# Performance work log

Hardware: AMD Instinct MI355X
Metric: run time of the kernel (lower is better)

Reference implementation:

```python
import jax, jax.numpy as jnp
import numpy as np
import math

N0, E, D_IN, H, NC, UH = 4096, 65536, 128, 256, 10, 64
K1 = math.ceil(0.8 * N0)   # 3277 nodes kept by pool1
K2 = math.ceil(0.2 * K1)   # 656 nodes kept by pool2

PARAM_SHAPES = dict(
    gcn1_w=(D_IN, H), gcn1_b=(H,), pool1_w=(H,), gcn2_w=(H, H), gcn2_b=(H,), pool2_w=(H,),
    inr_w=(H, H), inr_b=(H,), ini_w=(H, H), ini_b=(H,),
    enc1_w=(1, UH), enc1_b=(UH,), enc2_w=(UH, UH), enc2_b=(UH,),
    p1_w=(UH, UH), p1_b=(UH,), p2_w=(UH, UH // 2), p2_b=(UH // 2,),
    p3_w=(UH // 2, K2 * K2), p3_b=(K2 * K2,),
    rt_w=(H, H), rt_b=(H,), it_w=(H, H), it_b=(H,),
    msg_wr=(H, H), msg_wi=(H, H),
    mc1_w=(H, H // 2), mc1_b=(H // 2,), mc2_w=(H // 2, NC), mc2_b=(NC,),
    pc1_w=(H, H // 2), pc1_b=(H // 2,), pc2_w=(H // 2, NC), pc2_b=(NC,),
)

def gcn_conv(x, src, dst, emask, W, b):
    # GCNConv: self-loops + symmetric normalization; emask zeroes edges dropped by pooling
    n = x.shape[0]
    h = x @ W
    deg = jnp.zeros((n,), h.dtype).at[dst].add(emask) + 1.0
    dis = jax.lax.rsqrt(deg)
    coef = dis[src] * dis[dst] * emask
    out = jnp.zeros_like(h).at[dst].add(coef[:, None] * h[src])
    out = out + (dis * dis)[:, None] * h   # self-loop contribution
    return out + b

def topk_pool(x, src, dst, emask, w, k):
    # PyG TopKPooling: score = x@w/||w||, keep top-k, x <- x[perm]*tanh(score[perm])
    n = x.shape[0]
    score = (x @ w) / jnp.linalg.norm(w)
    _, perm = jax.lax.top_k(score, k)
    x_new = x[perm] * jnp.tanh(score[perm])[:, None]
    mapping = jnp.full((n,), -1, jnp.int32).at[perm].set(jnp.arange(k, dtype=jnp.int32))
    ns, nd = mapping[src], mapping[dst]
    nm = emask * (ns >= 0) * (nd >= 0)
    return x_new, jnp.maximum(ns, 0), jnp.maximum(nd, 0), nm

def herm_sqrt(C):
    C = (C + C.conj().T) * 0.5
    w, V = jnp.linalg.eigh(C)
    w = jnp.maximum(w, 0.0)
    return (V * jnp.sqrt(w + 1e-8)) @ V.conj().T

def forward(x, edge_index, P):
    src, dst = edge_index[0], edge_index[1]
    em = jnp.ones((src.shape[0],), jnp.float32)
    h = jax.nn.relu(gcn_conv(x, src, dst, em, P['gcn1_w'], P['gcn1_b']))
    h, src, dst, em = topk_pool(h, src, dst, em, P['pool1_w'], K1)
    h = jax.nn.relu(gcn_conv(h, src, dst, em, P['gcn2_w'], P['gcn2_b']))
    h, src, dst, em = topk_pool(h, src, dst, em, P['pool2_w'], K2)
    xr = h @ P['inr_w'] + P['inr_b']
    xi = h @ P['ini_w'] + P['ini_b']
    # --- LocalQuantumLayer (eval mode: dropout is identity) ---
    # ImprovedUnitaryDilationNetwork on the pooled graph (N = K2)
    xg = jnp.ones((K2, 1), jnp.float32)
    xg = jax.nn.relu(gcn_conv(xg, src, dst, em, P['enc1_w'], P['enc1_b']))
    xg = gcn_conv(xg, src, dst, em, P['enc2_w'], P['enc2_b'])
    emb = xg.mean(0)                                     # global_mean_pool, single graph
    t = jax.nn.relu(emb @ P['p1_w'] + P['p1_b'])
    t = jax.nn.relu(t @ P['p2_w'] + P['p2_b'])
    pm = jnp.tanh(t @ P['p3_w'] + P['p3_b']).reshape(K2, K2)
    A = 0.05 * ((pm - pm.T) * 0.5 + 1j * (pm + pm.T) * 0.5)  # antihermitian, scaled
    U = jax.scipy.linalg.expm(A)
    I = jnp.eye(K2, dtype=U.dtype)
    S1 = jax.lax.stop_gradient(herm_sqrt(I - U.conj().T @ U))
    S2 = jax.lax.stop_gradient(herm_sqrt(I - U @ U.conj().T))
    U_dil = jnp.concatenate([jnp.concatenate([U, S1], 1),
                             jnp.concatenate([S2, -U.conj().T], 1)], 0)
    xrt = jax.nn.relu(xr @ P['rt_w'] + P['rt_b'])
    xit = jax.nn.relu(xi @ P['it_w'] + P['it_b'])
    xc = xrt + 1j * xit
    # unitary_dim = 2*K2 > K2 nodes -> single batch, U_sub = U_dil[:K2,:K2]
    evolved = U_dil[:K2, :K2] @ xc
    Wm = P['msg_wr'] + 1j * P['msg_wi']
    msg = evolved[src] @ Wm                              # message(x_j) = x_j @ W (complex)
    agg = jnp.zeros_like(xc).at[dst].add(msg * em[:, None])  # aggr='add'
    outc = agg + (xr + 1j * xi)                          # identity residual (dims equal)
    mag = jnp.abs(outc)
    ph = jnp.arctan2(outc.imag, outc.real)
    gm, gp = mag.mean(0), ph.mean(0)                     # global_mean_pool, single graph
    lm = jax.nn.relu(gm @ P['mc1_w'] + P['mc1_b']) @ P['mc2_w'] + P['mc2_b']
    lp = jax.nn.relu(gp @ P['pc1_w'] + P['pc1_b']) @ P['pc2_w'] + P['pc2_b']
    return lm + lp

def setup_inputs() -> dict:
    key = jax.random.key(0)
    ks = iter(jax.random.split(key, 64))
    inp = {}
    inp['x'] = jax.random.normal(next(ks), (N0, D_IN), jnp.float32)
    inp['edge_index'] = jax.random.randint(next(ks), (2, E), 0, N0)
    for name, shp in PARAM_SHAPES.items():
        inp[name] = jax.random.normal(next(ks), shp, jnp.float32) * 0.05
    return inp

def reference(x, edge_index, gcn1_w, gcn1_b, pool1_w, gcn2_w, gcn2_b, pool2_w, inr_w, inr_b, ini_w, ini_b, enc1_w, enc1_b, enc2_w, enc2_b, p1_w, p1_b, p2_w, p2_b, p3_w, p3_b, rt_w, rt_b, it_w, it_b, msg_wr, msg_wi, mc1_w, mc1_b, mc2_w, mc2_b, pc1_w, pc1_b, pc2_w, pc2_b):
    P = dict(locals())
    x_ = P.pop('x'); ei = P.pop('edge_index')
    return forward(x_, ei, P)
```

## Files before the change

kernel.cpp:

```cpp
#include <hip/hip_runtime.h>
#include <cstddef>
#include <utility>

constexpr int N0  = 4096;
constexpr int E   = 65536;
constexpr int DIN = 128;
constexpr int HD  = 256;
constexpr int NC  = 10;
constexpr int UHD = 64;
constexpr int K1  = 3277;
constexpr int K2  = 656;
constexpr int PMN = K2 * K2;

constexpr int SQ_SLOTS = 4;

constexpr int PLD = 704;
constexpr size_t PPS = (size_t)PLD * PLD;

constexpr int CSPLIT = 8;

#define F4(n) ((size_t)(n) * 4)
constexpr size_t O_H1    = 0;
constexpr size_t O_OUT1  = O_H1    + F4(N0 * HD);
constexpr size_t O_DEG1  = O_OUT1  + F4(N0 * HD);
constexpr size_t O_DIS1  = O_DEG1  + F4(N0);
constexpr size_t O_SC1   = O_DIS1  + F4(N0);
constexpr size_t O_PERM1 = O_SC1   + F4(N0);
constexpr size_t O_MAP1  = O_PERM1 + F4(N0);
constexpr size_t O_H1P   = O_MAP1  + F4(N0);
constexpr size_t O_SRC2  = O_H1P   + F4(K1 * HD);
constexpr size_t O_DST2  = O_SRC2  + F4(E);
constexpr size_t O_EM2   = O_DST2  + F4(E);
constexpr size_t O_H2    = O_EM2   + F4(E);
constexpr size_t O_OUT2  = O_H2    + F4(K1 * HD);
constexpr size_t O_DEG2  = O_OUT2  + F4(K1 * HD);
constexpr size_t O_DIS2  = O_DEG2  + F4(N0);
constexpr size_t O_SC2   = O_DIS2  + F4(N0);
constexpr size_t O_PERM2 = O_SC2   + F4(N0);
constexpr size_t O_MAP2  = O_PERM2 + F4(N0);
constexpr size_t O_H2P   = O_MAP2  + F4(N0);
constexpr size_t O_SRC3  = O_H2P   + F4(K2 * HD);
constexpr size_t O_DST3  = O_SRC3  + F4(E);
constexpr size_t O_EM3   = O_DST3  + F4(E);
constexpr size_t O_XR    = O_EM3   + F4(E);
constexpr size_t O_XI    = O_XR    + F4(K2 * HD);
constexpr size_t O_DEG3  = O_XI    + F4(K2 * HD);
constexpr size_t O_DIS3  = O_DEG3  + F4(1024);
constexpr size_t O_SCOEF = O_DIS3  + F4(1024);
constexpr size_t O_XG1   = O_SCOEF + F4(1024);
constexpr size_t O_XG2H  = O_XG1   + F4(K2 * UHD);
constexpr size_t O_XG2   = O_XG2H  + F4(K2 * UHD);
constexpr size_t O_EMB   = O_XG2   + F4(K2 * UHD);
constexpr size_t O_T1    = O_EMB   + F4(64);
constexpr size_t O_T2    = O_T1    + F4(64);
constexpr size_t O_NORM  = O_T2    + F4(64);
constexpr size_t O_PM    = O_NORM  + F4(64);
constexpr size_t O_BM    = O_PM    + F4(PMN);
constexpr size_t O_P0    = O_BM    + F4(PMN) * 2;
constexpr size_t O_P1    = O_P0    + F4(PMN) * 2;
constexpr size_t O_XRT   = O_P1    + F4(PMN) * 2;
constexpr size_t O_XIT   = O_XRT   + F4(K2 * HD);
constexpr size_t O_XC    = O_XIT   + F4(K2 * HD);
constexpr size_t O_EVO   = O_XC    + F4(K2 * HD) * 2;
constexpr size_t O_AGG0  = O_EVO   + F4(K2 * HD) * 2;
constexpr size_t O_WC    = O_AGG0  + F4(K2 * HD) * 2;
constexpr size_t O_AGG1  = O_WC    + F4(HD * HD) * 2;
constexpr size_t O_MAG   = O_AGG1  + F4(K2 * HD) * 2;
constexpr size_t O_PH    = O_MAG   + F4(K2 * HD);
constexpr size_t O_GM    = O_PH    + F4(K2 * HD);
constexpr size_t O_GP    = O_GM    + F4(256);
constexpr size_t O_HM    = O_GP    + F4(256);
constexpr size_t O_HP    = O_HM    + F4(256);
constexpr size_t O_LM    = O_HP    + F4(256);
constexpr size_t O_LP    = O_LM    + F4(64);
constexpr size_t WS_NEED = O_LP    + F4(64);

constexpr size_t O_SA = 0;
constexpr size_t O_ST = O_SA + PPS * 2 * 4;
static_assert(O_ST + PPS * 2 * 4 <= O_SRC3, "SA/ST must fit in dead region");

constexpr size_t O_B2 = O_XRT;
static_assert(O_B2 + F4(PMN) * 2 <= O_MAG, "B2 must fit in XRT..AGG1 region");

constexpr size_t O_CSR_OFF = O_MAG;
constexpr size_t O_CSR_CUR = O_CSR_OFF + F4(4104);
constexpr size_t O_CSR_SRC = O_CSR_CUR + F4(4104);
constexpr size_t O_CSR_CF  = O_CSR_SRC + F4(E);
static_assert(O_CSR_CF + F4(E) <= O_GM, "CSR must fit in MAG/PH region");

constexpr size_t O_PARTX  = (WS_NEED + 255) & ~(size_t)255;
constexpr size_t PART_SZ  = (size_t)CSPLIT * PMN * 8;
constexpr size_t WS_TOTAL = O_PARTX + PART_SZ;

typedef __attribute__((ext_vector_type(8))) short s8v;
typedef __attribute__((ext_vector_type(4))) float f4v;

__device__ inline unsigned short f2bf(float x) {
  unsigned u = __float_as_uint(x);
  u += 0x7FFFu + ((u >> 16) & 1u);
  return (unsigned short)(u >> 16);
}
__device__ inline float bf2f(unsigned short h) {
  return __uint_as_float(((unsigned)h) << 16);
}
__device__ inline void split4(float re, float im, unsigned short* out,
                              size_t ps, size_t o) {
  unsigned short rh = f2bf(re);
  unsigned short rl = f2bf(re - bf2f(rh));
  unsigned short ih = f2bf(im);
  unsigned short il = f2bf(im - bf2f(ih));
  out[o] = rh; out[ps + o] = rl; out[2 * ps + o] = ih; out[3 * ps + o] = il;
}


template <int ACT>
__global__ void rmm64(const float* __restrict__ A, const float* __restrict__ B,
                      const float* __restrict__ bias, float* __restrict__ C,
                      int M, int N, int K, int CS, int CO) {
  __shared__ float As[64][17];
  __shared__ float Bs[16][64];
  int t  = threadIdx.x;
  int tx = t & 15, ty = t >> 4;
  int bm = blockIdx.y * 64, bn = blockIdx.x * 64;
  float ra[4], rb[4];
#pragma unroll
  for (int i = 0; i < 4; i++) {
    int l = t + i * 256;
    int gr = bm + (l >> 4);
    ra[i] = (gr < M) ? A[(size_t)gr * K + (l & 15)] : 0.f;
    int gc = bn + (l & 63);
    rb[i] = (gc < N) ? B[(size_t)(l >> 6) * N + gc] : 0.f;
  }
  float acc[4][4] = {};
  for (int kt = 0; kt < K; kt += 16) {
#pragma unroll
    for (int i = 0; i < 4; i++) {
      int l = t + i * 256;
      As[l >> 4][l & 15] = ra[i];
      Bs[l >> 6][l & 63] = rb[i];
    }
    __syncthreads();
    int kn = kt + 16;
    if (kn < K) {
#pragma unroll
      for (int i = 0; i < 4; i++) {
        int l = t + i * 256;
        int gr = bm + (l >> 4);
        ra[i] = (gr < M) ? A[(size_t)gr * K + kn + (l & 15)] : 0.f;
        int gc = bn + (l & 63);
        rb[i] = (gc < N) ? B[(size_t)(kn + (l >> 6)) * N + gc] : 0.f;
      }
    }
#pragma unroll
    for (int kk = 0; kk < 16; kk++) {
      float a[4], b[4];
#pragma unroll
      for (int i = 0; i < 4; i++) a[i] = As[ty + 16 * i][kk];
#pragma unroll
      for (int j = 0; j < 4; j++) b[j] = Bs[kk][tx + 16 * j];
#pragma unroll
      for (int i = 0; i < 4; i++)
#pragma unroll
        for (int j = 0; j < 4; j++) acc[i][j] += a[i] * b[j];
    }
    __syncthreads();
  }
#pragma unroll
  for (int i = 0; i < 4; i++) {
    int r = bm + ty + 16 * i;
    if (r >= M) continue;
#pragma unroll
    for (int j = 0; j < 4; j++) {
      int c = bn + tx + 16 * j;
      if (c >= N) continue;
      float v = acc[i][j] + (bias ? bias[c] : 0.f);
      if (ACT == 1) v = fmaxf(v, 0.f);
      C[((size_t)r * N + c) * CS + CO] = v;
    }
  }
}

template <int ACT>
__global__ void rmm64_dual(const float* __restrict__ A0, const float* __restrict__ A1,
                           const float* __restrict__ B0, const float* __restrict__ B1,
                           const float* __restrict__ b0, const float* __restrict__ b1,
                           float* __restrict__ C0, float* __restrict__ C1,
                           int M, int N, int K, int CS) {
  const float* A = blockIdx.z ? A1 : A0;
  const float* B = blockIdx.z ? B1 : B0;
  const float* bias = blockIdx.z ? b1 : b0;
  float* C = blockIdx.z ? C1 : C0;
  __shared__ float As[64][17];
  __shared__ float Bs[16][64];
  int t  = threadIdx.x;
  int tx = t & 15, ty = t >> 4;
  int bm = blockIdx.y * 64, bn = blockIdx.x * 64;
  float ra[4], rb[4];
#pragma unroll
  for (int i = 0; i < 4; i++) {
    int l = t + i * 256;
    int gr = bm + (l >> 4);
    ra[i] = (gr < M) ? A[(size_t)gr * K + (l & 15)] : 0.f;
    int gc = bn + (l & 63);
    rb[i] = (gc < N) ? B[(size_t)(l >> 6) * N + gc] : 0.f;
  }
  float acc[4][4] = {};
  for (int kt = 0; kt < K; kt += 16) {
#pragma unroll
    for (int i = 0; i < 4; i++) {
      int l = t + i * 256;
      As[l >> 4][l & 15] = ra[i];
      Bs[l >> 6][l & 63] = rb[i];
    }
    __syncthreads();
    int kn = kt + 16;
    if (kn < K) {
#pragma unroll
      for (int i = 0; i < 4; i++) {
        int l = t + i * 256;
        int gr = bm + (l >> 4);
        ra[i] = (gr < M) ? A[(size_t)gr * K + kn + (l & 15)] : 0.f;
        int gc = bn + (l & 63);
        rb[i] = (gc < N) ? B[(size_t)(kn + (l >> 6)) * N + gc] : 0.f;
      }
    }
#pragma unroll
    for (int kk = 0; kk < 16; kk++) {
      float a[4], b[4];
#pragma unroll
      for (int i = 0; i < 4; i++) a[i] = As[ty + 16 * i][kk];
#pragma unroll
      for (int j = 0; j < 4; j++) b[j] = Bs[kk][tx + 16 * j];
#pragma unroll
      for (int i = 0; i < 4; i++)
#pragma unroll
        for (int j = 0; j < 4; j++) acc[i][j] += a[i] * b[j];
    }
    __syncthreads();
  }
#pragma unroll
  for (int i = 0; i < 4; i++) {
    int r = bm + ty + 16 * i;
    if (r >= M) continue;
#pragma unroll
    for (int j = 0; j < 4; j++) {
      int c = bn + tx + 16 * j;
      if (c >= N) continue;
      float v = acc[i][j] + (bias ? bias[c] : 0.f);
      if (ACT == 1) v = fmaxf(v, 0.f);
      C[((size_t)r * N + c) * CS] = v;
    }
  }
}

__global__ void split_planesT(const float2* __restrict__ in, int inM, int inN,
                              unsigned short* __restrict__ out, int padR, int ld,
                              size_t ps) {
  __shared__ float2 tile[32][33];
  int tx = threadIdx.x & 31, ty = threadIdx.x >> 5;
  int k0 = blockIdx.x * 32, n0 = blockIdx.y * 32;
  for (int i = ty; i < 32; i += 8) {
    int k = k0 + i, n = n0 + tx;
    tile[i][tx] = (k < inM && n < inN) ? in[(size_t)k * inN + n]
                                       : make_float2(0.f, 0.f);
  }
  __syncthreads();
  for (int i = ty; i < 32; i += 8) {
    int n = n0 + i, k = k0 + tx;
    if (n < padR && k < ld)
      split4(tile[tx][i].x, tile[tx][i].y, out, ps, (size_t)n * ld + k);
  }
}

__global__ void split_planesT2(const float* __restrict__ re, const float* __restrict__ im,
                               int inM, int inN, unsigned short* __restrict__ out,
                               int padR, int ld, size_t ps) {
  __shared__ float2 tile[32][33];
  int tx = threadIdx.x & 31, ty = threadIdx.x >> 5;
  int k0 = blockIdx.x * 32, n0 = blockIdx.y * 32;
  for (int i = ty; i < 32; i += 8) {
    int k = k0 + i, n = n0 + tx;
    tile[i][tx] = (k < inM && n < inN)
        ? make_float2(re[(size_t)k * inN + n], im[(size_t)k * inN + n])
        : make_float2(0.f, 0.f);
  }
  __syncthreads();
  for (int i = ty; i < 32; i += 8) {
    int n = n0 + i, k = k0 + tx;
    if (n < padR && k < ld)
      split4(tile[tx][i].x, tile[tx][i].y, out, ps, (size_t)n * ld + k);
  }
}

__global__ __launch_bounds__(256, 2) void cmm_bf16_sk(
    const unsigned short* __restrict__ SA, size_t psA, int ldA,
    const unsigned short* __restrict__ ST, size_t psT, int ldT,
    float2* __restrict__ Part, int M, int N, int Kp, int chunk,
    const int* __restrict__ gate, int slot) {
  if (gate && slot >= *gate - 1) return;
  int k0 = blockIdx.x * chunk;
  int kend = min(Kp, k0 + chunk);
  int t = threadIdx.x;
  int wave = t >> 6, lane = t & 63;
  int quad = lane >> 4, mn = lane & 15;
  int rowA = blockIdx.z * 64 + wave * 16 + mn;
  int bn = blockIdx.y * 64;
  const unsigned short* a0 = SA + (size_t)rowA * ldA;
  f4v accR[4], accI[4];
#pragma unroll
  for (int i = 0; i < 4; i++) {
    accR[i] = (f4v){0.f, 0.f, 0.f, 0.f};
    accI[i] = (f4v){0.f, 0.f, 0.f, 0.f};
  }
  s8v cA[4], cB[4][4], nA[4], nB[4][4];
  {
    int ka = k0 + quad * 8;
#pragma unroll
    for (int p = 0; p < 4; p++) cA[p] = *(const s8v*)(a0 + p * psA + ka);
#pragma unroll
    for (int tl = 0; tl < 4; tl++) {
      const unsigned short* b0 = ST + (size_t)(bn + tl * 16 + mn) * ldT + ka;
#pragma unroll
      for (int p = 0; p < 4; p++) cB[tl][p] = *(const s8v*)(b0 + p * psT);
    }
  }
  for (int kt = k0; kt < kend; kt += 32) {
    int kn = kt + 32;
    if (kn < kend) {
      int ka = kn + quad * 8;
#pragma unroll
      for (int p = 0; p < 4; p++) nA[p] = *(const s8v*)(a0 + p * psA + ka);
#pragma unroll
      for (int tl = 0; tl < 4; tl++) {
        const unsigned short* b0 = ST + (size_t)(bn + tl * 16 + mn) * ldT + ka;
#pragma unroll
        for (int p = 0; p < 4; p++) nB[tl][p] = *(const s8v*)(b0 + p * psT);
      }
    }
    s8v nih, nil_;
#pragma unroll
    for (int q = 0; q < 8; q++) {
      nih[q]  = (short)(cA[2][q] ^ (short)0x8000);
      nil_[q] = (short)(cA[3][q] ^ (short)0x8000);
    }
#pragma unroll
    for (int tl = 0; tl < 4; tl++) {
      f4v r = accR[tl];
      r = __builtin_amdgcn_mfma_f32_16x16x32_bf16(cA[0], cB[tl][0], r, 0, 0, 0);
      r = __builtin_amdgcn_mfma_f32_16x16x32_bf16(cA[1], cB[tl][0], r, 0, 0, 0);
      r = __builtin_amdgcn_mfma_f32_16x16x32_bf16(cA[0], cB[tl][1], r, 0, 0, 0);
      r = __builtin_amdgcn_mfma_f32_16x16x32_bf16(nih, cB[tl][2], r, 0, 0, 0);
      r = __builtin_amdgcn_mfma_f32_16x16x32_bf16(nil_, cB[tl][2], r, 0, 0, 0);
      r = __builtin_amdgcn_mfma_f32_16x16x32_bf16(nih, cB[tl][3], r, 0, 0, 0);
      accR[tl] = r;
      f4v im = accI[tl];
      im = __builtin_amdgcn_mfma_f32_16x16x32_bf16(cA[0], cB[tl][2], im, 0, 0, 0);
      im = __builtin_amdgcn_mfma_f32_16x16x32_bf16(cA[1], cB[tl][2], im, 0, 0, 0);
      im = __builtin_amdgcn_mfma_f32_16x16x32_bf16(cA[0], cB[tl][3], im, 0, 0, 0);
      im = __builtin_amdgcn_mfma_f32_16x16x32_bf16(cA[2], cB[tl][0], im, 0, 0, 0);
      im = __builtin_amdgcn_mfma_f32_16x16x32_bf16(cA[3], cB[tl][0], im, 0, 0, 0);
      im = __builtin_amdgcn_mfma_f32_16x16x32_bf16(cA[2], cB[tl][1], im, 0, 0, 0);
      accI[tl] = im;
    }
    if (kn < kend) {
#pragma unroll
      for (int p = 0; p < 4; p++) cA[p] = nA[p];
#pragma unroll
      for (int tl = 0; tl < 4; tl++)
#pragma unroll
        for (int p = 0; p < 4; p++) cB[tl][p] = nB[tl][p];
    }
  }
  float2* P = Part + (size_t)blockIdx.x * M * N;
#pragma unroll
  for (int tl = 0; tl < 4; tl++) {
    int col = bn + tl * 16 + mn;
    if (col >= N) continue;
#pragma unroll
    for (int r = 0; r < 4; r++) {
      int row = blockIdx.z * 64 + wave * 16 + quad * 4 + r;
      if (row >= M) continue;
      P[(size_t)row * N + col] = make_float2(accR[tl][r], accI[tl][r]);
    }
  }
}

__global__ void creduce(const float2* __restrict__ Part, float2* __restrict__ C,
                        int MN, int N, int S, float e0,
                        const float2* __restrict__ E1, float e1,
                        const float2* __restrict__ E2, float e2) {
  int idx = blockIdx.x * 256 + threadIdx.x;
  if (idx >= MN) return;
  float sr = 0.f, si = 0.f;
  for (int z = 0; z < S; z++) {
    float2 p = Part[(size_t)z * MN + idx];
    sr += p.x;
    si += p.y;
  }
  if (e0 != 0.f) {
    int r = idx / N;
    if (idx - r * N == r) sr += e0;
  }
  if (E1) { float2 b = E1[idx]; sr += e1 * b.x; si += e1 * b.y; }
  if (E2) { float2 b = E2[idx]; sr += e2 * b.x; si += e2 * b.y; }
  C[idx] = make_float2(sr, si);
}

template <int WC_, int WSA, int WST>
__global__ void creduce_tiled(const float2* __restrict__ Part, int S, int M, int N,
                              int RP, int CP, float2* __restrict__ C,
                              unsigned short* __restrict__ SAp, size_t psA,
                              unsigned short* __restrict__ STp, size_t psT,
                              float e0, const float2* __restrict__ E1, float e1,
                              const float2* __restrict__ E2, float e2,
                              const int* __restrict__ gate, int slot) {
  if (gate && slot >= *gate - 1) return;
  __shared__ float vr[32][33], vi[32][33];
  int tx = threadIdx.x & 31, ty = threadIdx.x >> 5;
  int r0 = blockIdx.y * 32, c0 = blockIdx.x * 32;
  size_t MN = (size_t)M * N;
  for (int i = ty; i < 32; i += 8) {
    int r = r0 + i, c = c0 + tx;
    float sr = 0.f, si = 0.f;
    if (r < M && c < N) {
      size_t o = (size_t)r * N + c;
      for (int z = 0; z < S; z++) {
        float2 p = Part[z * MN + o];
        sr += p.x;
        si += p.y;
      }
      if (e0 != 0.f && r == c) sr += e0;
      if (E1) { float2 b = E1[o]; sr += e1 * b.x; si += e1 * b.y; }
      if (E2) { float2 b = E2[o]; sr += e2 * b.x; si += e2 * b.y; }
      if (WC_) C[o] = make_float2(sr, si);
    }
    if (WSA) split4(sr, si, SAp, psA, (size_t)r * CP + c);
    if (WST) { vr[i][tx] = sr; vi[i][tx] = si; }
  }
  if (WST) {
    __syncthreads();
    for (int i = ty; i < 32; i += 8) {
      int c = c0 + i, r = r0 + tx;
      split4(vr[tx][i], vi[tx][i], STp, psT, (size_t)c * RP + r);
    }
  }
}

__global__ void build_B_split(const float* __restrict__ pm, int n,
                              const float* __restrict__ scale_p,
                              float2* __restrict__ BM,
                              unsigned short* __restrict__ SAp,
                              unsigned short* __restrict__ STp, size_t ps,
                              int RP, int CP) {
  __shared__ float vr[32][33], vi[32][33];
  float scale = scale_p[0];
  int tx = threadIdx.x & 31, ty = threadIdx.x >> 5;
  int r0 = blockIdx.y * 32, c0 = blockIdx.x * 32;
  for (int i = ty; i < 32; i += 8) {
    int r = r0 + i, c = c0 + tx;
    float sr = 0.f, si = 0.f;
    if (r < n && c < n) {
      float pij = pm[(size_t)r * n + c];
      float pji = pm[(size_t)c * n + r];
      sr = scale * (pij - pji);
      si = scale * (pij + pji);
      BM[(size_t)r * n + c] = make_float2(sr, si);
    }
    split4(sr, si, SAp, ps, (size_t)r * CP + c);
    vr[i][tx] = sr;
    vi[i][tx] = si;
  }
  __syncthreads();
  for (int i = ty; i < 32; i += 8) {
    int c = c0 + i, r = r0 + tx;
    split4(vr[tx][i], vi[tx][i], STp, ps, (size_t)c * RP + r);
  }
}

__global__ void anorm_rows(const float* __restrict__ pm, int n,
                           int* __restrict__ anrm, int* __restrict__ done,
                           int* __restrict__ sdev, float* __restrict__ scale) {
  int i = blockIdx.x;
  __shared__ float red[256];
  float s = 0.f;
  for (int j = threadIdx.x; j < n; j += 256) {
    float pij = pm[(size_t)i * n + j];
    float pji = pm[(size_t)j * n + i];
    float a = pij - pji, b = pij + pji;
    s += sqrtf(a * a + b * b);
  }
  red[threadIdx.x] = s;
  __syncthreads();
  for (int off = 128; off > 0; off >>= 1) {
    if (threadIdx.x < off) red[threadIdx.x] += red[threadIdx.x + off];
    __syncthreads();
  }
  if (threadIdx.x == 0) {
    atomicMax(anrm, __float_as_int(red[0] * 0.025f));
    __threadfence();
    int d = atomicAdd(done, 1);
    if (d == gridDim.x - 1) {
      float a = __int_as_float(atomicMax(anrm, 0));
      int sq = (int)ceilf(log2f(fmaxf(a, 1e-20f) / 1.4f));
      sq = min(max(sq, 1), SQ_SLOTS + 1);
      *sdev = sq;
      *scale = 0.025f * exp2f(-(float)sq);
    }
  }
}

__global__ void combo3_planes(const float2* __restrict__ Bp, const float2* __restrict__ B2p,
                              unsigned short* __restrict__ planes, size_t ps,
                              int M, int N, int padR, int ld,
                              float e0, float e1, float e2) {
  int idx = blockIdx.x * 256 + threadIdx.x;
  if (idx >= padR * ld) return;
  int r = idx / ld, c = idx - r * ld;
  float sr = 0.f, si = 0.f;
  if (r < M && c < N) {
    size_t o = (size_t)r * N + c;
    float2 b = Bp[o], b2 = B2p[o];
    sr = e1 * b.x + e2 * b2.x;
    si = e1 * b.y + e2 * b2.y;
    if (r == c) sr += e0;
  }
  split4(sr, si, planes, ps, idx);
}

__global__ void hist_edges(const int* __restrict__ dst, const float* __restrict__ em,
                           int* __restrict__ cnt) {
  int e = blockIdx.x * 256 + threadIdx.x;
  if (e >= E) return;
  float m = em ? em[e] : 1.0f;
  if (m != 0.f) atomicAdd(&cnt[dst[e]], 1);
}

__global__ __launch_bounds__(1024) void scan_offsets(const int* __restrict__ cnt, int n,
                                                     int* __restrict__ off,
                                                     int* __restrict__ cur,
                                                     float* __restrict__ dis) {
  __shared__ int sums[1024];
  int t = threadIdx.x;
  int base = t * 4;
  int v[4];
  int s = 0;
#pragma unroll
  for (int j = 0; j < 4; j++) {
    int i = base + j;
    int ci = (i < n) ? cnt[i] : 0;
    if (i < n) dis[i] = 1.0f / sqrtf((float)ci + 1.0f);
    v[j] = s;
    s += ci;
  }
  sums[t] = s;
  __syncthreads();
  for (int d = 1; d < 1024; d <<= 1) {
    int x = (t >= d) ? sums[t - d] : 0;
    __syncthreads();
    sums[t] += x;
    __syncthreads();
  }
  int pre = (t > 0) ? sums[t - 1] : 0;
#pragma unroll
  for (int j = 0; j < 4; j++) {
    int i = base + j;
    if (i < n) { int o = pre + v[j]; off[i] = o; cur[i] = o; }
  }
  if (t == 1023) off[n] = sums[1023];
}

__global__ void fill_edges(const int* __restrict__ src, const int* __restrict__ dst,
                           const float* __restrict__ em, const float* __restrict__ dis,
                           int* __restrict__ cur, int* __restrict__ esrc,
                           float* __restrict__ ecoef) {
  int e = blockIdx.x * 256 + threadIdx.x;
  if (e >= E) return;
  float m = em ? em[e] : 1.0f;
  if (m == 0.f) return;
  int s = src[e], d = dst[e];
  int pos = atomicAdd(&cur[d], 1);
  esrc[pos] = s;
  ecoef[pos] = dis[s] * dis[d];
}

template <int ACT, int SCORE>
__global__ void gcn_gather(const int* __restrict__ off, const int* __restrict__ esrc,
                           const float* __restrict__ ecoef, const float* __restrict__ Hm,
                           const float* __restrict__ dis, const float* __restrict__ bias,
                           float* __restrict__ out, int F, int M,
                           const float* __restrict__ w, float* __restrict__ score,
                           float* __restrict__ normout) {
  __shared__ float red[256];
  int i = blockIdx.x;
  if (SCORE && i == M) {
    float s = 0.f;
    for (int k = threadIdx.x; k < F; k += 256) s += w[k] * w[k];
    red[threadIdx.x] = s;
    __syncthreads();
    for (int o = 128; o > 0; o >>= 1) {
      if (threadIdx.x < o) red[threadIdx.x] += red[threadIdx.x + o];
      __syncthreads();
    }
    if (threadIdx.x == 0) normout[0] = sqrtf(red[0]);
    return;
  }
  int e0 = off[i], e1 = off[i + 1];
  float d2 = dis[i] * dis[i];
  float sdot = 0.f;
  for (int f = threadIdx.x; f < F; f += blockDim.x) {
    float acc = d2 * Hm[(size_t)i * F + f] + bias[f];
    for (int e = e0; e < e1; e++)
      acc += ecoef[e] * Hm[(size_t)esrc[e] * F + f];
    if (ACT == 1) acc = fmaxf(acc, 0.f);
    out[(size_t)i * F + f] = acc;
    if (SCORE) sdot += acc * w[f];
  }
  if (SCORE) {
    red[threadIdx.x] = sdot;
    __syncthreads();
    for (int o = 128; o > 0; o >>= 1) {
      if (threadIdx.x < o) red[threadIdx.x] += red[threadIdx.x + o];
      __syncthreads();
    }
    if (threadIdx.x == 0) score[i] = red[0];
  }
}

__global__ void enc1_fused(const int* __restrict__ off, const float* __restrict__ ecoef,
                           const float* __restrict__ dis, const float* __restrict__ w,
                           const float* __restrict__ b, float* __restrict__ xg1) {
  int i = blockIdx.x;
  int lane = threadIdx.x;
  float s = 0.f;
  for (int e = off[i] + lane; e < off[i + 1]; e += 64) s += ecoef[e];
#pragma unroll
  for (int d = 32; d > 0; d >>= 1) s += __shfl_xor(s, d, 64);
  float sc = s + dis[i] * dis[i];
  xg1[(size_t)i * UHD + lane] = fmaxf(sc * w[lane] + b[lane], 0.f);
}

__global__ void agg_gather_split(const int* __restrict__ off, const int* __restrict__ esrc,
                                 const float2* __restrict__ evo,
                                 unsigned short* __restrict__ planes, size_t ps,
                                 int F, int M) {
  int i = blockIdx.x;
  if (i >= M) {
    for (int f = threadIdx.x; f < F; f += blockDim.x)
      split4(0.f, 0.f, planes, ps, (size_t)i * F + f);
    return;
  }
  int e0 = off[i], e1 = off[i + 1];
  for (int f = threadIdx.x; f < F; f += blockDim.x) {
    float sr = 0.f, si = 0.f;
    for (int e = e0; e < e1; e++) {
      float2 v = evo[(size_t)esrc[e] * F + f];
      sr += v.x;
      si += v.y;
    }
    split4(sr, si, planes, ps, (size_t)i * F + f);
  }
}

__global__ __launch_bounds__(1024) void bitonic_topk(const float* __restrict__ score,
                                                     int n, int* __restrict__ perm, int k,
                                                     int* __restrict__ map,
                                                     int* __restrict__ cntz, int ncnt) {
  __shared__ unsigned long long keys[4096];
  int t = threadIdx.x;
  for (int i = t; i < 4096; i += 1024) {
    unsigned long long kk = 0ull;
    if (i < n) {
      float f = score[i];
      unsigned u = __float_as_uint(f);
      u = (f >= 0.0f) ? (u | 0x80000000u) : ~u;
      kk = ((unsigned long long)u << 32) | (unsigned)(~(unsigned)i);
    }
    keys[i] = kk;
  }
  __syncthreads();
  for (int size = 2; size <= 4096; size <<= 1) {
    for (int stride = size >> 1; stride > 0; stride >>= 1) {
      for (int i = t; i < 2048; i += 1024) {
        int pos = ((i & ~(stride - 1)) << 1) | (i & (stride - 1));
        int partner = pos + stride;
        bool desc = (pos & size) == 0;
        unsigned long long a = keys[pos], b = keys[partner];
        if ((a < b) == desc) { keys[pos] = b; keys[partner] = a; }
      }
      __syncthreads();
    }
  }
  for (int i = t; i < 4096; i += 1024) {
    int idx = (int)(~(unsigned)(keys[i] & 0xFFFFFFFFull));
    if (idx >= 0) map[idx] = (i < k) ? i : -1;
    if (i < k) perm[i] = idx;
  }
  for (int i = t; i < ncnt; i += 1024) cntz[i] = 0;
}

__global__ void pool_remap(const float* __restrict__ X, const int* __restrict__ perm,
                           const float* __restrict__ dot, const float* __restrict__ normbuf,
                           float* __restrict__ Xn, int F, int k,
                           const int* __restrict__ srcIn, const int* __restrict__ dstIn,
                           const float* __restrict__ emIn, const int* __restrict__ map,
                           int* __restrict__ srcOut, int* __restrict__ dstOut,
                           float* __restrict__ emOut, int* __restrict__ cnt) {
  int b = blockIdx.x;
  if (b < k) {
    int p = perm[b];
    float sc = tanhf(dot[p] / normbuf[0]);
    for (int f = threadIdx.x; f < F; f += blockDim.x)
      Xn[(size_t)b * F + f] = X[(size_t)p * F + f] * sc;
  } else {
    int e = (b - k) * 256 + threadIdx.x;
    if (e >= E) return;
    int ns = map[srcIn[e]], nd = map[dstIn[e]];
    float m = emIn ? emIn[e] : 1.0f;
    if (ns < 0 || nd < 0) m = 0.f;
    srcOut[e] = ns < 0 ? 0 : ns;
    dstOut[e] = nd < 0 ? 0 : nd;
    emOut[e] = m;
    if (m != 0.f) atomicAdd(&cnt[nd], 1);
  }
}

__global__ void col_mean(const float* __restrict__ X, float* __restrict__ out,
                         int rows, int cols) {
  int c = blockIdx.x;
  __shared__ float red[256];
  float s = 0.f;
  for (int r = threadIdx.x; r < rows; r += 256) s += X[(size_t)r * cols + c];
  red[threadIdx.x] = s;
  __syncthreads();
  for (int off = 128; off > 0; off >>= 1) {
    if (threadIdx.x < off) red[threadIdx.x] += red[threadIdx.x + off];
    __syncthreads();
  }
  if (threadIdx.x == 0) out[c] = red[0] / (float)rows;
}

__global__ void magph_mean_part(const float2* __restrict__ Part, int S,
                                const float* __restrict__ xr,
                                const float* __restrict__ xi,
                                float* __restrict__ gm, float* __restrict__ gp,
                                int rows, int cols) {
  int c = blockIdx.x;
  __shared__ float rm[256], rp[256];
  size_t MN = (size_t)rows * cols;
  float sm = 0.f, sp = 0.f;
  for (int r = threadIdx.x; r < rows; r += 256) {
    size_t o = (size_t)r * cols + c;
    float re = xr[o], im = xi[o];
    for (int z = 0; z < S; z++) {
      float2 p = Part[z * MN + o];
      re += p.x;
      im += p.y;
    }
    sm += sqrtf(re * re + im * im);
    sp += atan2f(im, re);
  }
  rm[threadIdx.x] = sm;
  rp[threadIdx.x] = sp;
  __syncthreads();
  for (int off = 128; off > 0; off >>= 1) {
    if (threadIdx.x < off) {
      rm[threadIdx.x] += rm[threadIdx.x + off];
      rp[threadIdx.x] += rp[threadIdx.x + off];
    }
    __syncthreads();
  }
  if (threadIdx.x == 0) {
    gm[c] = rm[0] / (float)rows;
    gp[c] = rp[0] / (float)rows;
  }
}

__global__ void vecmat2(const float* __restrict__ v,
                        const float* __restrict__ W1, const float* __restrict__ b1,
                        const float* __restrict__ W2, const float* __restrict__ b2,
                        float* __restrict__ T2out) {
  __shared__ float vs[64], t1[64];
  int t = threadIdx.x;
  if (t < 64) vs[t] = v[t];
  __syncthreads();
  if (t < 64) {
    float acc = b1[t];
    for (int k = 0; k < 64; k++) acc += vs[k] * W1[(size_t)k * 64 + t];
    t1[t] = fmaxf(acc, 0.f);
  }
  __syncthreads();
  if (t < 32) {
    float acc = b2[t];
    for (int k = 0; k < 64; k++) acc += t1[k] * W2[(size_t)k * 32 + t];
    T2out[t] = fmaxf(acc, 0.f);
  }
}

__global__ void vecmat_tanh_wide(const float* __restrict__ v, const float* __restrict__ W,
                                 const float* __restrict__ b, float* __restrict__ out,
                                 int Kdim, int Ndim, int* __restrict__ anrm_init,
                                 int* __restrict__ done_init) {
  __shared__ float vs[64];
  if (threadIdx.x < Kdim) vs[threadIdx.x] = v[threadIdx.x];
  if (blockIdx.x == 0 && threadIdx.x == 0) { *anrm_init = 0; *done_init = 0; }
  __syncthreads();
  int j = blockIdx.x * 256 + threadIdx.x;
  if (j >= Ndim) return;
  float acc = b[j];
  for (int k = 0; k < Kdim; k++) acc += vs[k] * W[(size_t)k * Ndim + j];
  out[j] = tanhf(acc);
}

__global__ __launch_bounds__(256) void heads_fused(
    const float* __restrict__ GM, const float* __restrict__ GP,
    const float* __restrict__ mc1_w, const float* __restrict__ mc1_b,
    const float* __restrict__ mc2_w, const float* __restrict__ mc2_b,
    const float* __restrict__ pc1_w, const float* __restrict__ pc1_b,
    const float* __restrict__ pc2_w, const float* __restrict__ pc2_b,
    float* __restrict__ out) {
  __shared__ float g[256], h[128], acc[NC];
  int t = threadIdx.x;
  if (t < NC) acc[t] = 0.f;
  for (int pass = 0; pass < 2; pass++) {
    const float* gv = pass ? GP : GM;
    const float* w1 = pass ? pc1_w : mc1_w;
    const float* b1 = pass ? pc1_b : mc1_b;
    const float* w2 = pass ? pc2_w : mc2_w;
    const float* b2 = pass ? pc2_b : mc2_b;
    g[t] = gv[t];
    __syncthreads();
    if (t < 128) {
      float s = b1[t];
      for (int k = 0; k < 256; k++) s += g[k] * w1[(size_t)k * 128 + t];
      h[t] = fmaxf(s, 0.f);
    }
    __syncthreads();
    if (t < NC) {
      float s = b2[t];
      for (int k = 0; k < 128; k++) s += h[k] * w2[(size_t)k * NC + t];
      acc[t] += s;
    }
    __syncthreads();
  }
  if (t < NC) out[t] = acc[t];
}

static inline int sk_chunk32(int K, int S) { return (((K + S - 1) / S) + 31) & ~31; }

extern "C" void kernel_launch(void* const* d_in, const int* in_sizes, int n_in,
                              void* d_out, int out_size, void* d_ws, size_t ws_size,
                              hipStream_t stream) {
  if (ws_size < WS_TOTAL) return;

  const float* x       = (const float*)d_in[0];
  const int*   ei      = (const int*)d_in[1];
  const float* gcn1_w  = (const float*)d_in[2];
  const float* gcn1_b  = (const float*)d_in[3];
  const float* pool1_w = (const float*)d_in[4];
  const float* gcn2_w  = (const float*)d_in[5];
  const float* gcn2_b  = (const float*)d_in[6];
  const float* pool2_w = (const float*)d_in[7];
  const float* inr_w   = (const float*)d_in[8];
  const float* inr_b   = (const float*)d_in[9];
  const float* ini_w   = (const float*)d_in[10];
  const float* ini_b   = (const float*)d_in[11];
  const float* enc1_w  = (const float*)d_in[12];
  const float* enc1_b  = (const float*)d_in[13];
  const float* enc2_w  = (const float*)d_in[14];
  const float* enc2_b  = (const float*)d_in[15];
  const float* p1_w    = (const float*)d_in[16];
  const float* p1_b    = (const float*)d_in[17];
  const float* p2_w    = (const float*)d_in[18];
  const float* p2_b    = (const float*)d_in[19];
  const float* p3_w    = (const float*)d_in[20];
  const float* p3_b    = (const float*)d_in[21];
  const float* rt_w    = (const float*)d_in[22];
  const float* rt_b    = (const float*)d_in[23];
  const float* it_w    = (const float*)d_in[24];
  const float* it_b    = (const float*)d_in[25];
  const float* msg_wr  = (const float*)d_in[26];
  const float* msg_wi  = (const float*)d_in[27];
  const float* mc1_w   = (const float*)d_in[28];
  const float* mc1_b   = (const float*)d_in[29];
  const float* mc2_w   = (const float*)d_in[30];
  const float* mc2_b   = (const float*)d_in[31];
  const float* pc1_w   = (const float*)d_in[32];
  const float* pc1_b   = (const float*)d_in[33];
  const float* pc2_w   = (const float*)d_in[34];
  const float* pc2_b   = (const float*)d_in[35];

  char* ws = (char*)d_ws;
  float*  H1    = (float*)(ws + O_H1);
  float*  OUT1  = (float*)(ws + O_OUT1);
  int*    CNT1  = (int*)(ws + O_DEG1);
  float*  DIS1  = (float*)(ws + O_DIS1);
  float*  SC1   = (float*)(ws + O_SC1);
  int*    PERM1 = (int*)(ws + O_PERM1);
  int*    MAP1  = (int*)(ws + O_MAP1);
  float*  H1P   = (float*)(ws + O_H1P);
  int*    SRC2  = (int*)(ws + O_SRC2);
  int*    DST2  = (int*)(ws + O_DST2);
  float*  EM2   = (float*)(ws + O_EM2);
  float*  H2    = (float*)(ws + O_H2);
  float*  OUT2  = (float*)(ws + O_OUT2);
  int*    CNT2  = (int*)(ws + O_DEG2);
  float*  DIS2  = (float*)(ws + O_DIS2);
  float*  SC2   = (float*)(ws + O_SC2);
  int*    PERM2 = (int*)(ws + O_PERM2);
  int*    MAP2  = (int*)(ws + O_MAP2);
  float*  H2P   = (float*)(ws + O_H2P);
  int*    SRC3  = (int*)(ws + O_SRC3);
  int*    DST3  = (int*)(ws + O_DST3);
  float*  EM3   = (float*)(ws + O_EM3);
  float*  XRb   = (float*)(ws + O_XR);
  float*  XIb   = (float*)(ws + O_XI);
  int*    CNT3  = (int*)(ws + O_DEG3);
  float*  DIS3  = (float*)(ws + O_DIS3);
  float*  XG1   = (float*)(ws + O_XG1);
  float*  XG2H  = (float*)(ws + O_XG2H);
  float*  XG2   = (float*)(ws + O_XG2);
  float*  EMB   = (float*)(ws + O_EMB);
  float*  T2    = (float*)(ws + O_T2);
  float*  NORM  = (float*)(ws + O_NORM);
  int*    ANRM  = (int*)(NORM + 2);
  int*    SDEV  = (int*)(NORM + 3);
  float*  SCALE = NORM + 4;
  int*    DONE  = (int*)(NORM + 5);
  float*  PMV   = (float*)(ws + O_PM);
  float2* BM    = (float2*)(ws + O_BM);
  float2* XC    = (float2*)(ws + O_XC);
  float2* EVO   = (float2*)(ws + O_EVO);
  float*  GM    = (float*)(ws + O_GM);
  float*  GP    = (float*)(ws + O_GP);
  unsigned short* SA = (unsigned short*)(ws + O_SA);
  unsigned short* ST = (unsigned short*)(ws + O_ST);
  float2* PART  = (float2*)(ws + O_PARTX);
  float2* B2v   = (float2*)(ws + O_B2);
  int*    COFF  = (int*)(ws + O_CSR_OFF);
  int*    CCUR  = (int*)(ws + O_CSR_CUR);
  int*    CSRC  = (int*)(ws + O_CSR_SRC);
  float*  CCOEF = (float*)(ws + O_CSR_CF);

  const int* SRC1 = ei;
  const int* DST1 = ei + E;
  const int eg = E / 256;

  rmm64<0><<<dim3(HD / 64, N0 / 64), 256, 0, stream>>>(x, gcn1_w, nullptr, H1, N0, HD, DIN, 1, 0);
  hipMemsetAsync(CNT1, 0, F4(N0), stream);
  hist_edges<<<eg, 256, 0, stream>>>(DST1, nullptr, CNT1);
  scan_offsets<<<1, 1024, 0, stream>>>(CNT1, N0, COFF, CCUR, DIS1);
  fill_edges<<<eg, 256, 0, stream>>>(SRC1, DST1, nullptr, DIS1, CCUR, CSRC, CCOEF);
  gcn_gather<1, 1><<<N0 + 1, 256, 0, stream>>>(COFF, CSRC, CCOEF, H1, DIS1, gcn1_b,
                                               OUT1, HD, N0, pool1_w, SC1, NORM);

  bitonic_topk<<<1, 1024, 0, stream>>>(SC1, N0, PERM1, K1, MAP1, CNT2, K1);
  pool_remap<<<K1 + eg, 256, 0, stream>>>(OUT1, PERM1, SC1, NORM, H1P, HD, K1,
                                          SRC1, DST1, nullptr, MAP1, SRC2, DST2, EM2, CNT2);

  rmm64<0><<<dim3(HD / 64, (K1 + 63) / 64), 256, 0, stream>>>(H1P, gcn2_w, nullptr, H2, K1, HD, HD, 1, 0);
  scan_offsets<<<1, 1024, 0, stream>>>(CNT2, K1, COFF, CCUR, DIS2);
  fill_edges<<<eg, 256, 0, stream>>>(SRC2, DST2, EM2, DIS2, CCUR, CSRC, CCOEF);
  gcn_gather<1, 1><<<K1 + 1, 256, 0, stream>>>(COFF, CSRC, CCOEF, H2, DIS2, gcn2_b,
                                               OUT2, HD, K1, pool2_w, SC2, NORM + 1);

  bitonic_topk<<<1, 1024, 0, stream>>>(SC2, K1, PERM2, K2, MAP2, CNT3, K2);
  pool_remap<<<K2 + eg, 256, 0, stream>>>(OUT2, PERM2, SC2, NORM + 1, H2P, HD, K2,
                                          SRC2, DST2, EM2, MAP2, SRC3, DST3, EM3, CNT3);

  rmm64_dual<0><<<dim3(HD / 64, (K2 + 63) / 64, 2), 256, 0, stream>>>(
      H2P, H2P, inr_w, ini_w, inr_b, ini_b, XRb, XIb, K2, HD, HD, 1);

  scan_offsets<<<1, 1024, 0, stream>>>(CNT3, K2, COFF, CCUR, DIS3);
  fill_edges<<<eg, 256, 0, stream>>>(SRC3, DST3, EM3, DIS3, CCUR, CSRC, CCOEF);

  enc1_fused<<<K2, 64, 0, stream>>>(COFF, CCOEF, DIS3, enc1_w, enc1_b, XG1);
  rmm64<0><<<dim3(UHD / 64, (K2 + 63) / 64), 256, 0, stream>>>(XG1, enc2_w, nullptr, XG2H, K2, UHD, UHD, 1, 0);
  gcn_gather<0, 0><<<K2, 64, 0, stream>>>(COFF, CSRC, CCOEF, XG2H, DIS3, enc2_b,
                                          XG2, UHD, K2, nullptr, nullptr, nullptr);
  col_mean<<<UHD, 256, 0, stream>>>(XG2, EMB, K2, UHD);

  vecmat2<<<1, 64, 0, stream>>>(EMB, p1_w, p1_b, p2_w, p2_b, T2);
  vecmat_tanh_wide<<<(PMN + 255) / 256, 256, 0, stream>>>(T2, p3_w, p3_b, PMV, UHD / 2, PMN, ANRM, DONE);
  anorm_rows<<<K2, 256, 0, stream>>>(PMV, K2, ANRM, DONE, SDEV, SCALE);

  const int sgrid = (PLD * PLD + 255) / 256;
  const dim3 tg22(PLD / 32, PLD / 32);
  const int chF = sk_chunk32(PLD, CSPLIT);
  const dim3 gBig(CSPLIT, 11, 11);
  const float c3 = 1.f / 6.f, c4 = 1.f / 24.f, c5 = 1.f / 120.f;
  const float c6 = 1.f / 720.f, c7 = 1.f / 5040.f, c8 = 1.f / 40320.f;
  const float c9 = 1.f / 362880.f, c10 = 1.f / 3628800.f, c11 = 1.f / 39916800.f;

  build_B_split<<<tg22, 256, 0, stream>>>(PMV, K2, SCALE, BM, SA, ST, PPS, PLD, PLD);
  cmm_bf16_sk<<<gBig, 256, 0, stream>>>(SA, PPS, PLD, ST, PPS, PLD, PART, K2, K2, PLD, chF, nullptr, 0);
  creduce_tiled<1, 1, 0><<<tg22, 256, 0, stream>>>(PART, CSPLIT, K2, K2, PLD, PLD,
      B2v, SA, PPS, nullptr, 0, 0.f, nullptr, 0.f, nullptr, 0.f, nullptr, 0);
  cmm_bf16_sk<<<gBig, 256, 0, stream>>>(SA, PPS, PLD, ST, PPS, PLD, PART, K2, K2, PLD, chF, nullptr, 0);
  creduce_tiled<0, 0, 1><<<tg22, 256, 0, stream>>>(PART, CSPLIT, K2, K2, PLD, PLD,
      nullptr, nullptr, 0, ST, PPS, 0.f, nullptr, 0.f, nullptr, 0.f, nullptr, 0);
  combo3_planes<<<sgrid, 256, 0, stream>>>(BM, B2v, SA, PPS, K2, K2, PLD, PLD, c9, c10, c11);
  cmm_bf16_sk<<<gBig, 256, 0, stream>>>(SA, PPS, PLD, ST, PPS, PLD, PART, K2, K2, PLD, chF, nullptr, 0);
  creduce_tiled<0, 1, 0><<<tg22, 256, 0, stream>>>(PART, CSPLIT, K2, K2, PLD, PLD,
      nullptr, SA, PPS, nullptr, 0, c6, BM, c7, B2v, c8, nullptr, 0);
  cmm_bf16_sk<<<gBig, 256, 0, stream>>>(SA, PPS, PLD, ST, PPS, PLD, PART, K2, K2, PLD, chF, nullptr, 0);
  creduce_tiled<0, 1, 0><<<tg22, 256, 0, stream>>>(PART, CSPLIT, K2, K2, PLD, PLD,
      nullptr, SA, PPS, nullptr, 0, c3, BM, c4, B2v, c5, nullptr, 0);
  cmm_bf16_sk<<<gBig, 256, 0, stream>>>(SA, PPS, PLD, ST, PPS, PLD, PART, K2, K2, PLD, chF, nullptr, 0);
  creduce_tiled<0, 1, 1><<<tg22, 256, 0, stream>>>(PART, CSPLIT, K2, K2, PLD, PLD,
      nullptr, SA, PPS, ST, PPS, 1.f, BM, 1.f, B2v, 0.5f, nullptr, 0);
  for (int t = 0; t < SQ_SLOTS; ++t) {
    cmm_bf16_sk<<<gBig, 256, 0, stream>>>(SA, PPS, PLD, ST, PPS, PLD, PART, K2, K2, PLD, chF, SDEV, t);
    creduce_tiled<0, 1, 1><<<tg22, 256, 0, stream>>>(PART, CSPLIT, K2, K2, PLD, PLD,
        nullptr, SA, PPS, ST, PPS, 0.f, nullptr, 0.f, nullptr, 0.f, SDEV, t);
  }

  rmm64_dual<1><<<dim3(HD / 64, (K2 + 63) / 64, 2), 256, 0, stream>>>(
      XRb, XIb, rt_w, it_w, rt_b, it_b, (float*)XC, (float*)XC + 1, K2, HD, HD, 2);
  {
    const int mn = K2 * HD;
    const int rg = (mn + 255) / 256;
    const dim3 gSkin(CSPLIT, HD / 64, 11);
    const size_t psX = (size_t)HD * PLD;
    split_planesT<<<dim3((PLD + 31) / 32, (HD + 31) / 32), 256, 0, stream>>>(
        XC, K2, HD, ST, HD, PLD, psX);
    cmm_bf16_sk<<<gSkin, 256, 0, stream>>>(SA, PPS, PLD, ST, psX, PLD, PART, K2, HD, PLD, chF, nullptr, 0);
    creduce_tiled<0, 0, 1><<<dim3(HD / 32, PLD / 32), 256, 0, stream>>>(
        PART, CSPLIT, K2, HD, PLD, HD, nullptr, nullptr, 0, ST, psX,
        0.f, nullptr, 0.f, nullptr, 0.f, nullptr, 0);
    cmm_bf16_sk<<<gSkin, 256, 0, stream>>>(SA, PPS, PLD, ST, psX, PLD, PART, K2, HD, PLD, chF, nullptr, 0);
    creduce<<<rg, 256, 0, stream>>>(PART, EVO, mn, HD, CSPLIT, 0.f, nullptr, 0.f, nullptr, 0.f);
    const size_t psG = (size_t)PLD * HD;
    agg_gather_split<<<PLD, 256, 0, stream>>>(COFF, CSRC, EVO, SA, psG, HD, K2);
    split_planesT2<<<dim3((HD + 31) / 32, (HD + 31) / 32), 256, 0, stream>>>(
        msg_wr, msg_wi, HD, HD, ST, HD, HD, (size_t)HD * HD);
    cmm_bf16_sk<<<gSkin, 256, 0, stream>>>(SA, psG, HD, ST, (size_t)HD * HD, HD, PART,
                                           K2, HD, HD, sk_chunk32(HD, CSPLIT), nullptr, 0);
    magph_mean_part<<<HD, 256, 0, stream>>>(PART, CSPLIT, XRb, XIb, GM, GP, K2, HD);
  }

  heads_fused<<<1, 256, 0, stream>>>(GM, GP, mc1_w, mc1_b, mc2_w, mc2_b,
                                     pc1_w, pc1_b, pc2_w, pc2_b, (float*)d_out);
}
```

Before: 822.5 us.

## Stage shared B tile in LDS across waves in split-K complex bf16 GEMM

```diff
diff --git a/kernel.cpp b/kernel.cpp
--- a/kernel.cpp
+++ b/kernel.cpp
@@ -298,6 +298,7 @@
     float2* __restrict__ Part, int M, int N, int Kp, int chunk,
     const int* __restrict__ gate, int slot) {
   if (gate && slot >= *gate - 1) return;
+  __shared__ unsigned short Bl[2][4 * 64 * 32];
   int k0 = blockIdx.x * chunk;
   int kend = min(Kp, k0 + chunk);
   int t = threadIdx.x;
@@ -306,36 +307,36 @@
   int rowA = blockIdx.z * 64 + wave * 16 + mn;
   int bn = blockIdx.y * 64;
   const unsigned short* a0 = SA + (size_t)rowA * ldA;
+  int pB = t >> 6, cB_ = t & 63;
+  const unsigned short* bsrc = ST + (size_t)(bn + cB_) * ldT + pB * psT;
   f4v accR[4], accI[4];
 #pragma unroll
   for (int i = 0; i < 4; i++) {
     accR[i] = (f4v){0.f, 0.f, 0.f, 0.f};
     accI[i] = (f4v){0.f, 0.f, 0.f, 0.f};
   }
-  s8v cA[4], cB[4][4], nA[4], nB[4][4];
+  s8v cA[4], nA[4], rB[4], nB[4];
   {
     int ka = k0 + quad * 8;
 #pragma unroll
     for (int p = 0; p < 4; p++) cA[p] = *(const s8v*)(a0 + p * psA + ka);
 #pragma unroll
-    for (int tl = 0; tl < 4; tl++) {
-      const unsigned short* b0 = ST + (size_t)(bn + tl * 16 + mn) * ldT + ka;
-#pragma unroll
-      for (int p = 0; p < 4; p++) cB[tl][p] = *(const s8v*)(b0 + p * psT);
-    }
-  }
-  for (int kt = k0; kt < kend; kt += 32) {
+    for (int j = 0; j < 4; j++) rB[j] = *(const s8v*)(bsrc + k0 + j * 8);
+  }
+  int it = 0;
+  for (int kt = k0; kt < kend; kt += 32, ++it) {
+    int buf = it & 1;
+    unsigned short* bl = &Bl[buf][(size_t)t * 32];
+#pragma unroll
+    for (int j = 0; j < 4; j++) *(s8v*)(bl + j * 8) = rB[j];
+    __syncthreads();
     int kn = kt + 32;
     if (kn < kend) {
       int ka = kn + quad * 8;
 #pragma unroll
       for (int p = 0; p < 4; p++) nA[p] = *(const s8v*)(a0 + p * psA + ka);
 #pragma unroll
-      for (int tl = 0; tl < 4; tl++) {
-        const unsigned short* b0 = ST + (size_t)(bn + tl * 16 + mn) * ldT + ka;
-#pragma unroll
-        for (int p = 0; p < 4; p++) nB[tl][p] = *(const s8v*)(b0 + p * psT);
-      }
+      for (int j = 0; j < 4; j++) nB[j] = *(const s8v*)(bsrc + kn + j * 8);
     }
     s8v nih, nil_;
 #pragma unroll
@@ -345,30 +346,33 @@
     }
 #pragma unroll
     for (int tl = 0; tl < 4; tl++) {
+      int c = tl * 16 + mn;
+      s8v b0 = *(const s8v*)&Bl[buf][(0 * 64 + c) * 32 + quad * 8];
+      s8v b1 = *(const s8v*)&Bl[buf][(1 * 64 + c) * 32 + quad * 8];
+      s8v b2 = *(const s8v*)&Bl[buf][(2 * 64 + c) * 32 + quad * 8];
+      s8v b3 = *(const s8v*)&Bl[buf][(3 * 64 + c) * 32 + quad * 8];
       f4v r = accR[tl];
-      r = __builtin_amdgcn_mfma_f32_16x16x32_bf16(cA[0], cB[tl][0], r, 0, 0, 0);
-      r = __builtin_amdgcn_mfma_f32_16x16x32_bf16(cA[1], cB[tl][0], r, 0, 0, 0);
-      r = __builtin_amdgcn_mfma_f32_16x16x32_bf16(cA[0], cB[tl][1], r, 0, 0, 0);
-      r = __builtin_amdgcn_mfma_f32_16x16x32_bf16(nih, cB[tl][2], r, 0, 0, 0);
-      r = __builtin_amdgcn_mfma_f32_16x16x32_bf16(nil_, cB[tl][2], r, 0, 0, 0);
-      r = __builtin_amdgcn_mfma_f32_16x16x32_bf16(nih, cB[tl][3], r, 0, 0, 0);
+      r = __builtin_amdgcn_mfma_f32_16x16x32_bf16(cA[0], b0, r, 0, 0, 0);
+      r = __builtin_amdgcn_mfma_f32_16x16x32_bf16(cA[1], b0, r, 0, 0, 0);
+      r = __builtin_amdgcn_mfma_f32_16x16x32_bf16(cA[0], b1, r, 0, 0, 0);
+      r = __builtin_amdgcn_mfma_f32_16x16x32_bf16(nih, b2, r, 0, 0, 0);
+      r = __builtin_amdgcn_mfma_f32_16x16x32_bf16(nil_, b2, r, 0, 0, 0);
+      r = __builtin_amdgcn_mfma_f32_16x16x32_bf16(nih, b3, r, 0, 0, 0);
       accR[tl] = r;
       f4v im = accI[tl];
-      im = __builtin_amdgcn_mfma_f32_16x16x32_bf16(cA[0], cB[tl][2], im, 0, 0, 0);
-      im = __builtin_amdgcn_mfma_f32_16x16x32_bf16(cA[1], cB[tl][2], im, 0, 0, 0);
-      im = __builtin_amdgcn_mfma_f32_16x16x32_bf16(cA[0], cB[tl][3], im, 0, 0, 0);
-      im = __builtin_amdgcn_mfma_f32_16x16x32_bf16(cA[2], cB[tl][0], im, 0, 0, 0);
-      im = __builtin_amdgcn_mfma_f32_16x16x32_bf16(cA[3], cB[tl][0], im, 0, 0, 0);
-      im = __builtin_amdgcn_mfma_f32_16x16x32_bf16(cA[2], cB[tl][1], im, 0, 0, 0);
+      im = __builtin_amdgcn_mfma_f32_16x16x32_bf16(cA[0], b2, im, 0, 0, 0);
+      im = __builtin_amdgcn_mfma_f32_16x16x32_bf16(cA[1], b2, im, 0, 0, 0);
+      im = __builtin_amdgcn_mfma_f32_16x16x32_bf16(cA[0], b3, im, 0, 0, 0);
+      im = __builtin_amdgcn_mfma_f32_16x16x32_bf16(cA[2], b0, im, 0, 0, 0);
+      im = __builtin_amdgcn_mfma_f32_16x16x32_bf16(cA[3], b0, im, 0, 0, 0);
+      im = __builtin_amdgcn_mfma_f32_16x16x32_bf16(cA[2], b1, im, 0, 0, 0);
       accI[tl] = im;
     }
     if (kn < kend) {
 #pragma unroll
       for (int p = 0; p < 4; p++) cA[p] = nA[p];
 #pragma unroll
-      for (int tl = 0; tl < 4; tl++)
-#pragma unroll
-        for (int p = 0; p < 4; p++) cB[tl][p] = nB[tl][p];
+      for (int j = 0; j < 4; j++) rB[j] = nB[j];
     }
   }
   float2* P = Part + (size_t)blockIdx.x * M * N;
```

Result: faster. 731.3 us (median of 2 runs) (-11.1%).
